# Optimization experiments

Hardware: AMD Instinct MI355X
Metric: run time of the kernel (lower is better)

Reference implementation:

```python
import jax, jax.numpy as jnp
import numpy as np

DIM = 96
WS = 16            # window_size
OVERLAP = 0.5
UPSCALE = 2
NH = 1             # num_heads
OWIN = int(WS * OVERLAP) + WS          # 24, overlap_win_size
WSU = UPSCALE * WS                     # 32, window_size_up
TABLE = (WSU + OWIN - 1) ** 2          # 3025
PAD = (OWIN - WS) // 2                 # 4


def compute_rpi():
    # Faithful to calculate_rpi_owxra (incl. torch negative-index wraparound -> modulo).
    wsu, cur = WSU, WS + int(OVERLAP * WS)
    a = np.arange(wsu)
    coords_up = np.stack(np.meshgrid(a, a, indexing='ij')).reshape(2, -1)      # (2, wsu^2)
    b = np.arange(cur)
    coords_cur = np.stack(np.meshgrid(b, b, indexing='ij')).reshape(2, -1)     # (2, cur^2)
    rel = coords_cur[:, None, :] - coords_up[:, :, None]                       # (2, wsu^2, cur^2)
    rel = rel.transpose(1, 2, 0).astype(np.int64)
    rel += wsu - cur + 1
    rel[:, :, 0] *= wsu + cur - 1
    idx = rel.sum(-1) % TABLE                                                  # (wsu^2, cur^2)
    return jnp.asarray(idx)


def setup_inputs() -> dict:
    key = jax.random.key(0)
    ks = jax.random.split(key, 6)
    x = jax.random.normal(ks[0], (2, 128, 128, DIM), dtype=jnp.float32)
    x2 = jax.random.normal(ks[1], (128, WSU * WSU, DIM), dtype=jnp.float32)  # (b*nw, 1024, 96)
    Wkv = jax.random.normal(ks[2], (DIM, 2 * DIM), dtype=jnp.float32) * 0.02
    bkv = jnp.zeros((2 * DIM,), dtype=jnp.float32)
    bias_table = jax.random.normal(ks[3], (TABLE, NH), dtype=jnp.float32) * 0.02
    Wproj = jax.random.normal(ks[4], (DIM, DIM), dtype=jnp.float32) * 0.02
    bproj = jnp.zeros((DIM,), dtype=jnp.float32)
    return {"x": x, "x2": x2, "Wkv": Wkv, "bkv": bkv,
            "bias_table": bias_table, "Wproj": Wproj, "bproj": bproj}


def _forward(x, x2, Wkv, bkv, bias_table, Wproj, bproj, rpi):
    b, h, w, c = x.shape
    d = c // NH
    scale = d ** (-0.5)
    kv = x @ Wkv + bkv                                        # (b,h,w,2c); cols [:c]=k, [c:]=v
    p = jnp.pad(kv, ((0, 0), (PAD, PAD), (PAD, PAD), (0, 0)))
    nwh, nww = h // WS, w // WS
    idx_h = (jnp.arange(nwh) * WS)[:, None] + jnp.arange(OWIN)  # (nwh, OWIN)
    idx_w = (jnp.arange(nww) * WS)[:, None] + jnp.arange(OWIN)
    rows = p[:, idx_h]                                        # (b,nwh,OWIN,W',2c)
    wins = rows[:, :, :, idx_w]                               # (b,nwh,OWIN,nww,OWIN,2c)
    wins = wins.transpose(0, 1, 3, 2, 4, 5).reshape(b * nwh * nww, OWIN * OWIN, 2 * c)
    k = wins[..., :c]
    v = wins[..., c:]
    nwb, Q, _ = x2.shape
    K = OWIN * OWIN
    q = x2.reshape(nwb, Q, NH, d).transpose(0, 2, 1, 3) * scale   # (nwb,nh,Q,d)
    kh = k.reshape(nwb, K, NH, d).transpose(0, 2, 1, 3)
    vh = v.reshape(nwb, K, NH, d).transpose(0, 2, 1, 3)
    attn = jnp.einsum('bhqd,bhkd->bhqk', q, kh)
    bias = bias_table[rpi].transpose(2, 0, 1)                  # (nh,Q,K)
    attn = jax.nn.softmax(attn + bias[None], axis=-1)
    out = jnp.einsum('bhqk,bhkd->bhqd', attn, vh)
    out = out.transpose(0, 2, 1, 3).reshape(nwb, Q, c)
    return out @ Wproj + bproj


def reference(x, x2, Wkv, bkv, bias_table, Wproj, bproj):
    rpi = compute_rpi()
    return _forward(x, x2, Wkv, bkv, bias_table, Wproj, bproj, rpi)
```

## Files before the change

kernel.cpp:

```cpp
#include <hip/hip_runtime.h>
#include <hip/hip_bf16.h>
#include <stdint.h>

#define QLEN 1024
#define KLEN 576
#define TABLE_SZ 3025

typedef __attribute__((ext_vector_type(8))) short short8;
typedef __attribute__((ext_vector_type(4))) float floatx4;
typedef __attribute__((ext_vector_type(4))) unsigned short ushort4v;
typedef __attribute__((ext_vector_type(2))) int int2v;

static __device__ __forceinline__ unsigned short f2b(float f) {
    union { float f; unsigned int u; } v; v.f = f;
    return (unsigned short)((v.u + 0x7FFFu + ((v.u >> 16) & 1u)) >> 16);
}
static __device__ __forceinline__ int pk2(float lo, float hi) {
    union { __hip_bfloat162 h; int i; } u;
    u.h = __float22bfloat162_rn(float2{lo, hi});
    return u.i;
}
union W8 { unsigned int u[4]; short8 s8; };

static __device__ __forceinline__ short8 redist(int A, int B, int C, int D, bool godd) {
    int2v ef  = __builtin_amdgcn_permlane32_swap(A, C, false, false);
    int2v ebf = __builtin_amdgcn_permlane32_swap(B, D, false, false);
    int E = ef[0],  F = ef[1];
    int Eb = ebf[0], Fb = ebf[1];
    int E16 = __shfl_xor(E, 16), F16 = __shfl_xor(F, 16);
    int Eb16 = __shfl_xor(Eb, 16), Fb16 = __shfl_xor(Fb, 16);
    W8 w;
    w.u[0] = godd ? (unsigned)F16  : (unsigned)E;
    w.u[1] = godd ? (unsigned)Fb16 : (unsigned)Eb;
    w.u[2] = godd ? (unsigned)F    : (unsigned)E16;
    w.u[3] = godd ? (unsigned)Fb   : (unsigned)Eb16;
    return w.s8;
}

__global__ void prep_kernel(const float* __restrict__ Wkv, const float* __restrict__ Wproj,
                            const float* __restrict__ table,
                            unsigned short* __restrict__ WkvT, unsigned short* __restrict__ WprojT,
                            float* __restrict__ biasM) {
    const float LOG2E = 1.4426950408889634f;
    int t0 = blockIdx.x * blockDim.x + threadIdx.x;
    int stride = gridDim.x * blockDim.x;
    for (int i = t0; i < QLEN * KLEN; i += stride) {
        int qi = i / KLEN, kk = i - qi * KLEN;
        int rel0 = kk / 24 - qi / 32 + 9;
        int rel1 = kk % 24 - qi % 32 + 9;
        int s = rel0 * 55 + rel1;
        if (s < 0) s += TABLE_SZ;
        biasM[i] = table[s] * LOG2E;
    }
    for (int i = t0; i < 192 * 96; i += stride) {
        int n = i / 96, k = i - n * 96;
        WkvT[i] = f2b(Wkv[k * 192 + n]);
    }
    for (int i = t0; i < 96 * 96; i += stride) {
        int j = i / 96, d = i - j * 96;
        WprojT[i] = f2b(Wproj[d * 96 + j]);
    }
}

__global__ __launch_bounds__(256) void kv_kernel(const float* __restrict__ x,
        const unsigned short* __restrict__ WkvT, const float* __restrict__ bkv,
        unsigned short* __restrict__ Kpad, unsigned short* __restrict__ Vpad) {
    __shared__ unsigned short xt[64 * 104];
    __shared__ unsigned short vt2[96 * 72];
    int tid = threadIdx.x;
    int mbase = blockIdx.x * 64;
    int bb = mbase >> 14, rem = mbase & 16383;
    int hy = rem >> 7, hx0 = rem & 127;
    #pragma unroll
    for (int it = 0; it < 6; ++it) {
        int c = tid + it * 256;
        int row = c / 24, col4 = (c - row * 24) * 4;
        floatx4 v = *(const floatx4*)(x + (mbase + row) * 96 + col4);
        ushort4v o;
        o[0] = f2b(v[0]); o[1] = f2b(v[1]); o[2] = f2b(v[2]); o[3] = f2b(v[3]);
        *(ushort4v*)&xt[row * 104 + col4] = o;
    }
    __syncthreads();
    int lane = tid & 63, wv = tid >> 6;
    int g = lane >> 4, c16 = lane & 15;
    short8 a[3];
    #pragma unroll
    for (int c = 0; c < 3; ++c)
        a[c] = *(const short8*)&xt[(wv * 16 + c16) * 104 + c * 32 + g * 8];
    floatx4 acc[12];
    #pragma unroll
    for (int nt = 0; nt < 12; ++nt) acc[nt] = (floatx4){0.f, 0.f, 0.f, 0.f};
    #pragma unroll
    for (int nt = 0; nt < 12; ++nt)
        #pragma unroll
        for (int c = 0; c < 3; ++c) {
            short8 b = *(const short8*)(WkvT + (nt * 16 + c16) * 96 + c * 32 + g * 8);
            acc[nt] = __builtin_amdgcn_mfma_f32_16x16x32_bf16(a[c], b, acc[nt], 0, 0, 0);
        }
    #pragma unroll
    for (int nt = 0; nt < 6; ++nt) {
        int col = nt * 16 + c16;
        float bk = bkv[col];
        #pragma unroll
        for (int r = 0; r < 4; ++r) {
            int rowl = wv * 16 + g * 4 + r;
            Kpad[((bb * 136 + hy + 4) * 136 + hx0 + rowl + 4) * 96 + col] = f2b(acc[nt][r] + bk);
        }
    }
    #pragma unroll
    for (int nt = 6; nt < 12; ++nt) {
        int d = nt * 16 + c16 - 96;
        float bk = bkv[96 + d];
        #pragma unroll
        for (int r = 0; r < 4; ++r) {
            int rowl = wv * 16 + g * 4 + r;
            vt2[d * 72 + rowl] = f2b(acc[nt][r] + bk);
        }
    }
    __syncthreads();
    #pragma unroll
    for (int it = 0; it < 3; ++it) {
        int v = tid + it * 256;
        int d = v >> 3, ch = v & 7;
        short8 val = *(const short8*)&vt2[d * 72 + ch * 8];
        *(short8*)(Vpad + ((bb * 96 + d) * 136 + hy + 4) * 136 + hx0 + 4 + ch * 8) = val;
    }
}

__global__ __launch_bounds__(512, 4) void attn_kernel(const float* __restrict__ x2,
        const unsigned short* __restrict__ Kpad, const unsigned short* __restrict__ Vpad,
        const float* __restrict__ biasM,
        const unsigned short* __restrict__ WprojT, const float* __restrict__ bproj,
        float* __restrict__ out) {
    __shared__ unsigned short Kt[2][64 * 104];
    __shared__ unsigned short Vt[2][96 * 72];

    int bid_hw = blockIdx.x;
    int bid = (bid_hw & 7) * 128 + (bid_hw >> 3);
    int wb = bid >> 3, qb = bid & 7;
    int bb = wb >> 6, wy = (wb >> 3) & 7, wx = wb & 7;
    int tid = threadIdx.x, lane = tid & 63, wv = tid >> 6;
    int g = lane >> 4, c16 = lane & 15;
    int qlo = qb * 128 + wv * 16;
    bool godd = (lane & 16) != 0;

    const float qscale = 0.10206207261596577f * 1.4426950408889634f;
    short8 qf[3];
    #pragma unroll
    for (int c = 0; c < 3; ++c) {
        const float* src = x2 + (wb * 1024 + qlo + c16) * 96 + c * 32 + g * 8;
        floatx4 v0 = *(const floatx4*)src;
        floatx4 v1 = *(const floatx4*)(src + 4);
        short8 q;
        #pragma unroll
        for (int i = 0; i < 4; ++i) {
            q[i]     = (short)f2b(v0[i] * qscale);
            q[4 + i] = (short)f2b(v1[i] * qscale);
        }
        qf[c] = q;
    }

    short8 pre[3];
    auto loadpre = [&](int kt) {
        #pragma unroll
        for (int it = 0; it < 3; ++it) {
            int c = tid + it * 512;
            if (c < 768) {
                int kr = c / 12, part = c - kr * 12;
                int kk = kt * 64 + kr;
                int oh = kk / 24, ow = kk - oh * 24;
                pre[it] = *(const short8*)(Kpad + ((bb * 136 + wy * 16 + oh) * 136 + wx * 16 + ow) * 96 + part * 8);
            } else {
                int v = c - 768;
                int d = v >> 3, ch = v & 7;
                int kk0 = kt * 64 + ch * 8;
                int oh = kk0 / 24, ow0 = kk0 - oh * 24;
                pre[it] = *(const short8*)(Vpad + ((bb * 96 + d) * 136 + wy * 16 + oh) * 136 + wx * 16 + ow0);
            }
        }
    };
    auto store_buf = [&](int b) {
        #pragma unroll
        for (int it = 0; it < 3; ++it) {
            int c = tid + it * 512;
            if (c < 768) {
                int kr = c / 12, part = c - kr * 12;
                *(short8*)&Kt[b][kr * 104 + part * 8] = pre[it];
            } else {
                int v = c - 768;
                int d = v >> 3, ch = v & 7;
                *(short8*)&Vt[b][d * 72 + ch * 8] = pre[it];
            }
        }
    };

    floatx4 Oa[6];
    #pragma unroll
    for (int dt = 0; dt < 6; ++dt) Oa[dt] = (floatx4){0.f, 0.f, 0.f, 0.f};
    float lp = 0.f;

    loadpre(0);
    store_buf(0);
    loadpre(1);
    __syncthreads();

    for (int kt = 0; kt < 9; ++kt) {
        int cur = kt & 1;
        if (kt < 8) {
            store_buf(cur ^ 1);
            if (kt < 7) loadpre(kt + 2);
        }

        float sv[4][4];
        __builtin_amdgcn_s_setprio(1);
        #pragma unroll
        for (int sub = 0; sub < 4; ++sub) {
            floatx4 acc = (floatx4){0.f, 0.f, 0.f, 0.f};
            #pragma unroll
            for (int c = 0; c < 3; ++c) {
                short8 kf = *(const short8*)&Kt[cur][(sub * 16 + c16) * 104 + c * 32 + g * 8];
                acc = __builtin_amdgcn_mfma_f32_16x16x32_bf16(kf, qf[c], acc, 0, 0, 0);
            }
            floatx4 bv = *(const floatx4*)(biasM + (qlo + c16) * 576 + kt * 64 + sub * 16 + g * 4);
            #pragma unroll
            for (int r = 0; r < 4; ++r) {
                float p = __builtin_amdgcn_exp2f(acc[r] + bv[r]);
                sv[sub][r] = p;
                lp += p;
            }
        }
        __builtin_amdgcn_s_setprio(0);

        #pragma unroll
        for (int kc = 0; kc < 2; ++kc) {
            int A = pk2(sv[2 * kc][0], sv[2 * kc][1]);
            int B = pk2(sv[2 * kc][2], sv[2 * kc][3]);
            int C = pk2(sv[2 * kc + 1][0], sv[2 * kc + 1][1]);
            int D = pk2(sv[2 * kc + 1][2], sv[2 * kc + 1][3]);
            short8 pf = redist(A, B, C, D, godd);
            __builtin_amdgcn_s_setprio(1);
            #pragma unroll
            for (int dt = 0; dt < 6; ++dt) {
                short8 vf = *(const short8*)&Vt[cur][(dt * 16 + c16) * 72 + kc * 32 + g * 8];
                Oa[dt] = __builtin_amdgcn_mfma_f32_16x16x32_bf16(vf, pf, Oa[dt], 0, 0, 0);
            }
            __builtin_amdgcn_s_setprio(0);
        }

        __syncthreads();
    }

    float ts = lp;
    ts += __shfl_xor(ts, 16);
    ts += __shfl_xor(ts, 32);
    float inv = 1.0f / ts;
    int w2[6][2];
    #pragma unroll
    for (int dt = 0; dt < 6; ++dt) {
        w2[dt][0] = pk2(Oa[dt][0] * inv, Oa[dt][1] * inv);
        w2[dt][1] = pk2(Oa[dt][2] * inv, Oa[dt][3] * inv);
    }
    short8 of[3];
    #pragma unroll
    for (int kc = 0; kc < 3; ++kc)
        of[kc] = redist(w2[2 * kc][0], w2[2 * kc][1], w2[2 * kc + 1][0], w2[2 * kc + 1][1], godd);
    #pragma unroll
    for (int jt = 0; jt < 6; ++jt) {
        floatx4 acc = (floatx4){0.f, 0.f, 0.f, 0.f};
        #pragma unroll
        for (int kc = 0; kc < 3; ++kc) {
            short8 wf = *(const short8*)(WprojT + (jt * 16 + c16) * 96 + kc * 32 + g * 8);
            acc = __builtin_amdgcn_mfma_f32_16x16x32_bf16(of[kc], wf, acc, 0, 0, 0);
        }
        int col = jt * 16 + c16;
        float bp = bproj[col];
        #pragma unroll
        for (int r = 0; r < 4; ++r)
            out[(wb * 1024 + qlo + g * 4 + r) * 96 + col] = acc[r] + bp;
    }
}

extern "C" void kernel_launch(void* const* d_in, const int* in_sizes, int n_in,
                              void* d_out, int out_size, void* d_ws, size_t ws_size,
                              hipStream_t stream) {
    const float* x     = (const float*)d_in[0];
    const float* x2    = (const float*)d_in[1];
    const float* Wkv   = (const float*)d_in[2];
    const float* bkv   = (const float*)d_in[3];
    const float* table = (const float*)d_in[4];
    const float* Wproj = (const float*)d_in[5];
    const float* bproj = (const float*)d_in[6];
    float* out = (float*)d_out;

    char* ws = (char*)d_ws;
    unsigned short* Kpad   = (unsigned short*)ws;
    unsigned short* Vpad   = (unsigned short*)(ws + 7102464);
    float*          biasM  = (float*)(ws + 14204928);
    unsigned short* WkvT   = (unsigned short*)(ws + 16564224);
    unsigned short* WprojT = (unsigned short*)(ws + 16601088);

    hipMemsetAsync(ws, 0, 14204928, stream);
    hipLaunchKernelGGL(prep_kernel, dim3(512), dim3(256), 0, stream,
                       Wkv, Wproj, table, WkvT, WprojT, biasM);
    hipLaunchKernelGGL(kv_kernel, dim3(512), dim3(256), 0, stream,
                       x, WkvT, bkv, Kpad, Vpad);
    hipLaunchKernelGGL(attn_kernel, dim3(1024), dim3(512), 0, stream,
                       x2, Kpad, Vpad, biasM, WprojT, bproj, out);
}
```

Before: 100.5 us.

## Switch attention kernel to 32x32x16 MFMA with 32 queries per wave

The attention kernel moves from 16x16x32 to 32x32x16 bf16 MFMA tiles. Each wave now handles 32 query rows instead of 16, so the grid is halved and each K/V tile staged in LDS is reused across twice as many queries. The C-to-B fragment redistribution drops from permlane32_swap plus four shuffles and selects to just permlane32_swap. The cost is more accumulator registers per wave, so launch bounds are relaxed to 2 blocks, which lowers occupancy and leaves fewer blocks to spread across CUs.

```diff
diff --git a/kernel.cpp b/kernel.cpp
--- a/kernel.cpp
+++ b/kernel.cpp
@@ -8,6 +8,7 @@
 
 typedef __attribute__((ext_vector_type(8))) short short8;
 typedef __attribute__((ext_vector_type(4))) float floatx4;
+typedef __attribute__((ext_vector_type(16))) float floatx16;
 typedef __attribute__((ext_vector_type(4))) unsigned short ushort4v;
 typedef __attribute__((ext_vector_type(2))) int int2v;
 
@@ -22,18 +23,14 @@
 }
 union W8 { unsigned int u[4]; short8 s8; };
 
-static __device__ __forceinline__ short8 redist(int A, int B, int C, int D, bool godd) {
-    int2v ef  = __builtin_amdgcn_permlane32_swap(A, C, false, false);
-    int2v ebf = __builtin_amdgcn_permlane32_swap(B, D, false, false);
-    int E = ef[0],  F = ef[1];
-    int Eb = ebf[0], Fb = ebf[1];
-    int E16 = __shfl_xor(E, 16), F16 = __shfl_xor(F, 16);
-    int Eb16 = __shfl_xor(Eb, 16), Fb16 = __shfl_xor(Fb, 16);
+static __device__ __forceinline__ short8 bfrag(int w0, int w1, int w2, int w3) {
+    int2v pa = __builtin_amdgcn_permlane32_swap(w0, w2, false, false);
+    int2v pb = __builtin_amdgcn_permlane32_swap(w1, w3, false, false);
     W8 w;
-    w.u[0] = godd ? (unsigned)F16  : (unsigned)E;
-    w.u[1] = godd ? (unsigned)Fb16 : (unsigned)Eb;
-    w.u[2] = godd ? (unsigned)F    : (unsigned)E16;
-    w.u[3] = godd ? (unsigned)Fb   : (unsigned)Eb16;
+    w.u[0] = (unsigned)pa[0];
+    w.u[1] = (unsigned)pb[0];
+    w.u[2] = (unsigned)pa[1];
+    w.u[3] = (unsigned)pb[1];
     return w.s8;
 }
 
@@ -127,7 +124,7 @@
     }
 }
 
-__global__ __launch_bounds__(512, 4) void attn_kernel(const float* __restrict__ x2,
+__global__ __launch_bounds__(512, 2) void attn_kernel(const float* __restrict__ x2,
         const unsigned short* __restrict__ Kpad, const unsigned short* __restrict__ Vpad,
         const float* __restrict__ biasM,
         const unsigned short* __restrict__ WprojT, const float* __restrict__ bproj,
@@ -136,19 +133,18 @@
     __shared__ unsigned short Vt[2][96 * 72];
 
     int bid_hw = blockIdx.x;
-    int bid = (bid_hw & 7) * 128 + (bid_hw >> 3);
-    int wb = bid >> 3, qb = bid & 7;
+    int bid = (bid_hw & 7) * 64 + (bid_hw >> 3);
+    int wb = bid >> 2, qb = bid & 3;
     int bb = wb >> 6, wy = (wb >> 3) & 7, wx = wb & 7;
     int tid = threadIdx.x, lane = tid & 63, wv = tid >> 6;
-    int g = lane >> 4, c16 = lane & 15;
-    int qlo = qb * 128 + wv * 16;
-    bool godd = (lane & 16) != 0;
+    int l31 = lane & 31, h = lane >> 5;
+    int qlo = qb * 256 + wv * 32;
 
     const float qscale = 0.10206207261596577f * 1.4426950408889634f;
-    short8 qf[3];
-    #pragma unroll
-    for (int c = 0; c < 3; ++c) {
-        const float* src = x2 + (wb * 1024 + qlo + c16) * 96 + c * 32 + g * 8;
+    short8 qf[6];
+    #pragma unroll
+    for (int c = 0; c < 6; ++c) {
+        const float* src = x2 + (wb * 1024 + qlo + l31) * 96 + c * 16 + h * 8;
         floatx4 v0 = *(const floatx4*)src;
         floatx4 v1 = *(const floatx4*)(src + 4);
         short8 q;
@@ -194,9 +190,10 @@
         }
     };
 
-    floatx4 Oa[6];
-    #pragma unroll
-    for (int dt = 0; dt < 6; ++dt) Oa[dt] = (floatx4){0.f, 0.f, 0.f, 0.f};
+    floatx16 Oa[3];
+    #pragma unroll
+    for (int dt = 0; dt < 3; ++dt)
+        Oa[dt] = (floatx16){0.f,0.f,0.f,0.f,0.f,0.f,0.f,0.f,0.f,0.f,0.f,0.f,0.f,0.f,0.f,0.f};
     float lp = 0.f;
 
     loadpre(0);
@@ -211,38 +208,51 @@
             if (kt < 7) loadpre(kt + 2);
         }
 
-        float sv[4][4];
+        floatx16 s0 = (floatx16){0.f,0.f,0.f,0.f,0.f,0.f,0.f,0.f,0.f,0.f,0.f,0.f,0.f,0.f,0.f,0.f};
+        floatx16 s1 = s0;
         __builtin_amdgcn_s_setprio(1);
         #pragma unroll
-        for (int sub = 0; sub < 4; ++sub) {
-            floatx4 acc = (floatx4){0.f, 0.f, 0.f, 0.f};
-            #pragma unroll
-            for (int c = 0; c < 3; ++c) {
-                short8 kf = *(const short8*)&Kt[cur][(sub * 16 + c16) * 104 + c * 32 + g * 8];
-                acc = __builtin_amdgcn_mfma_f32_16x16x32_bf16(kf, qf[c], acc, 0, 0, 0);
-            }
-            floatx4 bv = *(const floatx4*)(biasM + (qlo + c16) * 576 + kt * 64 + sub * 16 + g * 4);
-            #pragma unroll
-            for (int r = 0; r < 4; ++r) {
-                float p = __builtin_amdgcn_exp2f(acc[r] + bv[r]);
-                sv[sub][r] = p;
-                lp += p;
-            }
+        for (int c = 0; c < 6; ++c) {
+            short8 kf0 = *(const short8*)&Kt[cur][l31 * 104 + c * 16 + h * 8];
+            short8 kf1 = *(const short8*)&Kt[cur][(32 + l31) * 104 + c * 16 + h * 8];
+            s0 = __builtin_amdgcn_mfma_f32_32x32x16_bf16(kf0, qf[c], s0, 0, 0, 0);
+            s1 = __builtin_amdgcn_mfma_f32_32x32x16_bf16(kf1, qf[c], s1, 0, 0, 0);
         }
         __builtin_amdgcn_s_setprio(0);
 
-        #pragma unroll
-        for (int kc = 0; kc < 2; ++kc) {
-            int A = pk2(sv[2 * kc][0], sv[2 * kc][1]);
-            int B = pk2(sv[2 * kc][2], sv[2 * kc][3]);
-            int C = pk2(sv[2 * kc + 1][0], sv[2 * kc + 1][1]);
-            int D = pk2(sv[2 * kc + 1][2], sv[2 * kc + 1][3]);
-            short8 pf = redist(A, B, C, D, godd);
+        const float* brow = biasM + (qlo + l31) * 576 + kt * 64 + h * 4;
+        int w[16];
+        #pragma unroll
+        for (int t = 0; t < 4; ++t) {
+            floatx4 bv = *(const floatx4*)(brow + t * 8);
+            float p0 = __builtin_amdgcn_exp2f(s0[4 * t + 0] + bv[0]);
+            float p1 = __builtin_amdgcn_exp2f(s0[4 * t + 1] + bv[1]);
+            float p2 = __builtin_amdgcn_exp2f(s0[4 * t + 2] + bv[2]);
+            float p3 = __builtin_amdgcn_exp2f(s0[4 * t + 3] + bv[3]);
+            lp += (p0 + p1) + (p2 + p3);
+            w[t * 2 + 0] = pk2(p0, p1);
+            w[t * 2 + 1] = pk2(p2, p3);
+        }
+        #pragma unroll
+        for (int t = 0; t < 4; ++t) {
+            floatx4 bv = *(const floatx4*)(brow + 32 + t * 8);
+            float p0 = __builtin_amdgcn_exp2f(s1[4 * t + 0] + bv[0]);
+            float p1 = __builtin_amdgcn_exp2f(s1[4 * t + 1] + bv[1]);
+            float p2 = __builtin_amdgcn_exp2f(s1[4 * t + 2] + bv[2]);
+            float p3 = __builtin_amdgcn_exp2f(s1[4 * t + 3] + bv[3]);
+            lp += (p0 + p1) + (p2 + p3);
+            w[8 + t * 2 + 0] = pk2(p0, p1);
+            w[8 + t * 2 + 1] = pk2(p2, p3);
+        }
+
+        #pragma unroll
+        for (int kc = 0; kc < 4; ++kc) {
+            short8 pf = bfrag(w[kc * 4 + 0], w[kc * 4 + 1], w[kc * 4 + 2], w[kc * 4 + 3]);
             __builtin_amdgcn_s_setprio(1);
             #pragma unroll
-            for (int dt = 0; dt < 6; ++dt) {
-                short8 vf = *(const short8*)&Vt[cur][(dt * 16 + c16) * 72 + kc * 32 + g * 8];
-                Oa[dt] = __builtin_amdgcn_mfma_f32_16x16x32_bf16(vf, pf, Oa[dt], 0, 0, 0);
+            for (int dt = 0; dt < 3; ++dt) {
+                short8 vf = *(const short8*)&Vt[cur][(dt * 32 + l31) * 72 + kc * 16 + h * 8];
+                Oa[dt] = __builtin_amdgcn_mfma_f32_32x32x16_bf16(vf, pf, Oa[dt], 0, 0, 0);
             }
             __builtin_amdgcn_s_setprio(0);
         }
@@ -250,33 +260,36 @@
         __syncthreads();
     }
 
-    float ts = lp;
-    ts += __shfl_xor(ts, 16);
-    ts += __shfl_xor(ts, 32);
-    float inv = 1.0f / ts;
-    int w2[6][2];
-    #pragma unroll
-    for (int dt = 0; dt < 6; ++dt) {
-        w2[dt][0] = pk2(Oa[dt][0] * inv, Oa[dt][1] * inv);
-        w2[dt][1] = pk2(Oa[dt][2] * inv, Oa[dt][3] * inv);
-    }
-    short8 of[3];
-    #pragma unroll
-    for (int kc = 0; kc < 3; ++kc)
-        of[kc] = redist(w2[2 * kc][0], w2[2 * kc][1], w2[2 * kc + 1][0], w2[2 * kc + 1][1], godd);
-    #pragma unroll
-    for (int jt = 0; jt < 6; ++jt) {
-        floatx4 acc = (floatx4){0.f, 0.f, 0.f, 0.f};
-        #pragma unroll
-        for (int kc = 0; kc < 3; ++kc) {
-            short8 wf = *(const short8*)(WprojT + (jt * 16 + c16) * 96 + kc * 32 + g * 8);
-            acc = __builtin_amdgcn_mfma_f32_16x16x32_bf16(of[kc], wf, acc, 0, 0, 0);
-        }
-        int col = jt * 16 + c16;
-        float bp = bproj[col];
-        #pragma unroll
-        for (int r = 0; r < 4; ++r)
-            out[(wb * 1024 + qlo + g * 4 + r) * 96 + col] = acc[r] + bp;
+    lp += __shfl_xor(lp, 32);
+    float inv = 1.0f / lp;
+    short8 of[6];
+    #pragma unroll
+    for (int dt = 0; dt < 3; ++dt) {
+        int ow[8];
+        #pragma unroll
+        for (int t = 0; t < 4; ++t) {
+            ow[t * 2 + 0] = pk2(Oa[dt][4 * t + 0] * inv, Oa[dt][4 * t + 1] * inv);
+            ow[t * 2 + 1] = pk2(Oa[dt][4 * t + 2] * inv, Oa[dt][4 * t + 3] * inv);
+        }
+        of[dt * 2 + 0] = bfrag(ow[0], ow[1], ow[2], ow[3]);
+        of[dt * 2 + 1] = bfrag(ow[4], ow[5], ow[6], ow[7]);
+    }
+    #pragma unroll
+    for (int jt = 0; jt < 3; ++jt) {
+        floatx16 acc = (floatx16){0.f,0.f,0.f,0.f,0.f,0.f,0.f,0.f,0.f,0.f,0.f,0.f,0.f,0.f,0.f,0.f};
+        #pragma unroll
+        for (int st = 0; st < 6; ++st) {
+            short8 wf = *(const short8*)(WprojT + (jt * 32 + l31) * 96 + st * 16 + h * 8);
+            acc = __builtin_amdgcn_mfma_f32_32x32x16_bf16(wf, of[st], acc, 0, 0, 0);
+        }
+        int row = wb * 1024 + qlo + l31;
+        #pragma unroll
+        for (int t = 0; t < 4; ++t) {
+            floatx4 bp = *(const floatx4*)(bproj + jt * 32 + t * 8 + h * 4);
+            #pragma unroll
+            for (int r = 0; r < 4; ++r)
+                out[row * 96 + jt * 32 + t * 8 + h * 4 + r] = acc[4 * t + r] + bp[r];
+        }
     }
 }
 
@@ -304,6 +317,6 @@
                        Wkv, Wproj, table, WkvT, WprojT, biasM);
     hipLaunchKernelGGL(kv_kernel, dim3(512), dim3(256), 0, stream,
                        x, WkvT, bkv, Kpad, Vpad);
-    hipLaunchKernelGGL(attn_kernel, dim3(1024), dim3(512), 0, stream,
+    hipLaunchKernelGGL(attn_kernel, dim3(512), dim3(512), 0, stream,
                        x2, Kpad, Vpad, biasM, WprojT, bproj, out);
 }
```

Result: slower. 111.7 us (+11.1%).
